# Kernel tuning notes

Measured on AMD Instinct MI355X. Metric: run time of the kernel, lower is better.

The kernel has to match this reference:

```python
import jax, jax.numpy as jnp
import numpy as np

N, D, K, MAX_ITER = 131072, 64, 512, 5


def setup_inputs() -> dict:
    key = jax.random.key(0)
    k1, k2, k3 = jax.random.split(key, 3)
    X = jax.random.normal(k1, (N, D), dtype=jnp.float32)
    centers = jax.random.normal(k2, (K, D), dtype=jnp.float32)
    repl_idx = jax.random.randint(k3, (MAX_ITER, K), 0, N, dtype=jnp.int32)
    return {"X": X, "centers": centers, "repl_idx": repl_idx}


def _assign(X, centers):
    # squared euclidean distance matrix [N, K]; argmin identical to cdist argmin
    x2 = jnp.sum(X * X, axis=1, keepdims=True)          # [N,1]
    c2 = jnp.sum(centers * centers, axis=1)             # [K]
    d2 = x2 + c2[None, :] - 2.0 * (X @ centers.T)       # [N,K]
    return jnp.argmin(d2, axis=1)


def reference(X, centers, repl_idx):
    n_clusters = centers.shape[0]
    assignments = None
    for i in range(MAX_ITER):
        assignments = _assign(X, centers)
        # scatter_mean: per-cluster sum / count (empty clusters -> 0, as torch_scatter)
        sums = jax.ops.segment_sum(X, assignments, num_segments=n_clusters)
        counts = jax.ops.segment_sum(jnp.ones((X.shape[0],), X.dtype), assignments,
                                     num_segments=n_clusters)
        new_centers = sums / jnp.maximum(counts, 1.0)[:, None]
        # re-initialize any exactly-zero entries from random data points
        new_centers_init = X[repl_idx[i]]                 # [K,D]
        new_centers = jnp.where(new_centers == 0, new_centers_init, new_centers)
        centers = new_centers
    return assignments, centers
```

## Files before the change

### kernel.cpp

```cpp
#include <hip/hip_runtime.h>

#define N_PTS 131072
#define KC    512
#define DIM   64
#define MAXIT 5
#define NCHUNK 64
#define CHUNK_PTS (N_PTS / NCHUNK)
#define FIXSCALE 1099511627776.0

typedef short v8s __attribute__((ext_vector_type(8)));
typedef float v4f __attribute__((ext_vector_type(4)));

__device__ __forceinline__ unsigned short bf16_rtne(float x) {
    unsigned int u = __float_as_uint(x);
    return (unsigned short)((u + 0x7FFFu + ((u >> 16) & 1u)) >> 16);
}
__device__ __forceinline__ float bf16_f32(unsigned short b) {
    return __uint_as_float(((unsigned int)b) << 16);
}
__device__ __forceinline__ void split3(float x, short& h, short& m, short& l) {
    unsigned short hb = bf16_rtne(x);
    float r1 = x - bf16_f32(hb);
    unsigned short mb = bf16_rtne(r1);
    float r2 = r1 - bf16_f32(mb);
    h = (short)hb; m = (short)mb; l = (short)bf16_rtne(r2);
}

__device__ __forceinline__ void gload_lds16(const unsigned short* g, void* lds) {
    __builtin_amdgcn_global_load_lds(
        (const __attribute__((address_space(1))) void*)g,
        (__attribute__((address_space(3))) void*)lds,
        16, 0, 0);
}

__global__ __launch_bounds__(256) void prep_kernel(
        const float* __restrict__ C, float* __restrict__ c2out,
        unsigned short* __restrict__ Ch, unsigned short* __restrict__ Cm,
        unsigned short* __restrict__ Cl) {
    int k = blockIdx.x * 256 + threadIdx.x;
    if (k < KC) {
        float sq[DIM];
        #pragma unroll
        for (int j = 0; j < DIM; ++j) {
            float c = C[k * DIM + j];
            sq[j] = c * c;
            short h, m, l;
            split3(c, h, m, l);
            Ch[k * DIM + j] = (unsigned short)h;
            Cm[k * DIM + j] = (unsigned short)m;
            Cl[k * DIM + j] = (unsigned short)l;
        }
        #pragma unroll
        for (int st = 1; st < DIM; st <<= 1)
            #pragma unroll
            for (int j = 0; j < DIM; j += 2 * st)
                sq[j] = sq[j] + sq[j + st];
        c2out[k] = sq[0];
    }
}

__global__ __launch_bounds__(256, 4) void assign_kernel(
        const float* __restrict__ X,
        const unsigned short* __restrict__ Ch,
        const unsigned short* __restrict__ Cm,
        const unsigned short* __restrict__ Cl,
        const float* __restrict__ c2v, float* __restrict__ out_f) {
    __shared__ __align__(16) short Bt[2 * 6 * 64 * 8];
    __shared__ float c2t[KC];
    __shared__ float x2p[4][2][16][8];
    __shared__ float x2f[4][2][16];

    const int t   = threadIdx.x;
    const int wv  = t >> 6;
    const int l   = t & 63;
    const int row = l & 15;
    const int q   = l >> 4;
    const int pbase = blockIdx.x * 128 + wv * 32;

    const unsigned short* const gsrc1 =
        ((wv < 2) ? Ch : Cm) + (size_t)(row * 64 + (wv & 1) * 32 + q * 8);
    const unsigned short* const gsrc2 =
        Cl + (size_t)(row * 64 + wv * 32 + q * 8);

    v8s* const BtV = (v8s*)Bt;
    v8s* const lds1 = BtV + wv * 64;
    v8s* const lds2 = BtV + 256 + wv * 64;

    gload_lds16(gsrc1, lds1);
    if (wv < 2) gload_lds16(gsrc2, lds2);

    for (int i = t; i < KC; i += 256) c2t[i] = c2v[i];

    v8s ah[2][2], am[2][2], al[2][2];
    #pragma unroll
    for (int T = 0; T < 2; ++T) {
        const float* xr = X + (size_t)(pbase + T * 16 + row) * DIM + q * 8;
        #pragma unroll
        for (int kc = 0; kc < 2; ++kc) {
            float4 v0 = *(const float4*)(xr + kc * 32);
            float4 v1 = *(const float4*)(xr + kc * 32 + 4);
            float e[8] = { v0.x, v0.y, v0.z, v0.w, v1.x, v1.y, v1.z, v1.w };
            v8s H, M, L;
            #pragma unroll
            for (int j = 0; j < 8; ++j) {
                short hh, mm, ll;
                split3(e[j], hh, mm, ll);
                H[j] = hh; M[j] = mm; L[j] = ll;
            }
            ah[T][kc] = H; am[T][kc] = M; al[T][kc] = L;
            float s0 = e[0]*e[0], s1 = e[1]*e[1], s2 = e[2]*e[2], s3 = e[3]*e[3];
            float s4 = e[4]*e[4], s5 = e[5]*e[5], s6 = e[6]*e[6], s7 = e[7]*e[7];
            x2p[wv][T][row][kc * 4 + q] =
                ((s0 + s1) + (s2 + s3)) + ((s4 + s5) + (s6 + s7));
        }
    }
    __syncthreads();
    if (t < 128) {
        int w2 = t >> 5, T2 = (t >> 4) & 1, pt = t & 15;
        const float* P = x2p[w2][T2][pt];
        x2f[w2][T2][pt] = ((P[0] + P[1]) + (P[2] + P[3]))
                        + ((P[4] + P[5]) + (P[6] + P[7]));
    }
    __syncthreads();
    float x2x[2][4];
    #pragma unroll
    for (int T = 0; T < 2; ++T)
        #pragma unroll
        for (int r = 0; r < 4; ++r)
            x2x[T][r] = x2f[wv][T][q * 4 + r];

    float bd[2][4];
    int   bk[2][4];
    #pragma unroll
    for (int T = 0; T < 2; ++T)
        #pragma unroll
        for (int r = 0; r < 4; ++r) { bd[T][r] = 3.4e38f; bk[T][r] = 0; }

    for (int ct = 0; ct < 32; ++ct) {
        const int cur = ct & 1;
        if (ct < 31) {
            const size_t goff = (size_t)(ct + 1) * 1024;
            gload_lds16(gsrc1 + goff, lds1 + (cur ^ 1) * 384);
            if (wv < 2) gload_lds16(gsrc2 + goff, lds2 + (cur ^ 1) * 384);
        }
        v8s* const rb = BtV + cur * 384;
        v8s bh0 = rb[0 * 64 + l];
        v8s bh1 = rb[1 * 64 + l];
        v8s bm0 = rb[2 * 64 + l];
        v8s bm1 = rb[3 * 64 + l];
        v8s bl0 = rb[4 * 64 + l];
        v8s bl1 = rb[5 * 64 + l];
        float c2k = c2t[ct * 16 + row];

        #pragma unroll
        for (int T = 0; T < 2; ++T) {
            v4f acc = {0.f, 0.f, 0.f, 0.f};
            acc = __builtin_amdgcn_mfma_f32_16x16x32_bf16(ah[T][0], bh0, acc, 0, 0, 0);
            acc = __builtin_amdgcn_mfma_f32_16x16x32_bf16(ah[T][1], bh1, acc, 0, 0, 0);
            acc = __builtin_amdgcn_mfma_f32_16x16x32_bf16(am[T][0], bh0, acc, 0, 0, 0);
            acc = __builtin_amdgcn_mfma_f32_16x16x32_bf16(am[T][1], bh1, acc, 0, 0, 0);
            acc = __builtin_amdgcn_mfma_f32_16x16x32_bf16(ah[T][0], bm0, acc, 0, 0, 0);
            acc = __builtin_amdgcn_mfma_f32_16x16x32_bf16(ah[T][1], bm1, acc, 0, 0, 0);
            acc = __builtin_amdgcn_mfma_f32_16x16x32_bf16(am[T][0], bm0, acc, 0, 0, 0);
            acc = __builtin_amdgcn_mfma_f32_16x16x32_bf16(am[T][1], bm1, acc, 0, 0, 0);
            acc = __builtin_amdgcn_mfma_f32_16x16x32_bf16(al[T][0], bh0, acc, 0, 0, 0);
            acc = __builtin_amdgcn_mfma_f32_16x16x32_bf16(al[T][1], bh1, acc, 0, 0, 0);
            acc = __builtin_amdgcn_mfma_f32_16x16x32_bf16(ah[T][0], bl0, acc, 0, 0, 0);
            acc = __builtin_amdgcn_mfma_f32_16x16x32_bf16(ah[T][1], bl1, acc, 0, 0, 0);
            #pragma unroll
            for (int r = 0; r < 4; ++r) {
                float tt = x2x[T][r] + c2k;
                float d2 = fmaf(-2.0f, acc[r], tt);
                if (d2 < bd[T][r]) { bd[T][r] = d2; bk[T][r] = ct * 16 + row; }
            }
        }
        if (ct < 31) __syncthreads();
    }

    #pragma unroll
    for (int T = 0; T < 2; ++T)
        #pragma unroll
        for (int r = 0; r < 4; ++r) {
            unsigned int b = __float_as_uint(bd[T][r]);
            b = (b & 0x80000000u) ? ~b : (b | 0x80000000u);
            unsigned long long key = ((unsigned long long)b << 32)
                                   | (unsigned int)bk[T][r];
            #pragma unroll
            for (int st = 1; st <= 8; st <<= 1) {
                unsigned long long o = __shfl_xor(key, st, 64);
                if (o < key) key = o;
            }
            if (row == 0) {
                int p = pbase + T * 16 + q * 4 + r;
                out_f[p] = (float)((int)(unsigned int)key);
            }
        }
}

__global__ __launch_bounds__(256) void accum_kernel(
        const float* __restrict__ X, const float* __restrict__ af,
        unsigned long long* __restrict__ qsums, int* __restrict__ counts) {
    __shared__ unsigned long long lsum[KC * 16];
    __shared__ int lcnt[KC];
    int slice = blockIdx.x & 3;
    int chunk = blockIdx.x >> 2;
    int p4 = threadIdx.x >> 2;
    int c4 = threadIdx.x & 3;

    for (int i = threadIdx.x; i < KC * 16; i += 256) lsum[i] = 0ull;
    for (int i = threadIdx.x; i < KC; i += 256) lcnt[i] = 0;
    __syncthreads();

    int base = chunk * CHUNK_PTS;
    #pragma unroll 2
    for (int it = 0; it < CHUNK_PTS / 64; ++it) {
        int n = base + it * 64 + p4;
        int a = (int)af[n];
        float4 xv = *(const float4*)(X + (size_t)n * DIM + slice * 16 + c4 * 4);
        long long q0 = (long long)llrint((double)xv.x * FIXSCALE);
        long long q1 = (long long)llrint((double)xv.y * FIXSCALE);
        long long q2 = (long long)llrint((double)xv.z * FIXSCALE);
        long long q3 = (long long)llrint((double)xv.w * FIXSCALE);
        atomicAdd(&lsum[a * 16 + c4 * 4 + 0], (unsigned long long)q0);
        atomicAdd(&lsum[a * 16 + c4 * 4 + 1], (unsigned long long)q1);
        atomicAdd(&lsum[a * 16 + c4 * 4 + 2], (unsigned long long)q2);
        atomicAdd(&lsum[a * 16 + c4 * 4 + 3], (unsigned long long)q3);
        if (slice == 0 && c4 == 0) atomicAdd(&lcnt[a], 1);
    }
    __syncthreads();

    for (int i = threadIdx.x; i < KC * 16; i += 256) {
        unsigned long long v = lsum[i];
        if (v != 0ull)
            atomicAdd(&qsums[(i >> 4) * DIM + slice * 16 + (i & 15)], v);
    }
    if (slice == 0)
        for (int i = threadIdx.x; i < KC; i += 256) {
            int v = lcnt[i];
            if (v != 0) atomicAdd(&counts[i], v);
        }
}

__global__ __launch_bounds__(256) void update_kernel(
        const unsigned long long* __restrict__ qsums,
        const int* __restrict__ counts,
        const int* __restrict__ repl, const float* __restrict__ X,
        float* __restrict__ outC, float* __restrict__ c2v,
        unsigned short* __restrict__ Ch, unsigned short* __restrict__ Cm,
        unsigned short* __restrict__ Cl) {
    int k = blockIdx.x * 4 + (threadIdx.x >> 6);
    int d = threadIdx.x & 63;

    long long qq = (long long)qsums[k * DIM + d];
    float s = (float)((double)qq * (1.0 / FIXSCALE));
    float cnt = (float)counts[k];
    float v = s / fmaxf(cnt, 1.0f);
    if (v == 0.0f) v = X[(size_t)repl[k] * DIM + d];
    outC[k * DIM + d] = v;

    short h, m, l;
    split3(v, h, m, l);
    Ch[k * DIM + d] = (unsigned short)h;
    Cm[k * DIM + d] = (unsigned short)m;
    Cl[k * DIM + d] = (unsigned short)l;

    float sq = v * v;
    #pragma unroll
    for (int st = 1; st < 64; st <<= 1)
        sq += __shfl_xor(sq, st, 64);
    if (d == 0) c2v[k] = sq;
}

extern "C" void kernel_launch(void* const* d_in, const int* in_sizes, int n_in,
                              void* d_out, int out_size, void* d_ws, size_t ws_size,
                              hipStream_t stream) {
    const float* X    = (const float*)d_in[0];
    const float* C0   = (const float*)d_in[1];
    const int*   repl = (const int*)d_in[2];
    float* out = (float*)d_out;

    char* ws = (char*)d_ws;
    unsigned short* Ch = (unsigned short*)(ws + 0);
    unsigned short* Cm = (unsigned short*)(ws + (64 << 10));
    unsigned short* Cl = (unsigned short*)(ws + (128 << 10));
    unsigned long long* qsums = (unsigned long long*)(ws + (192 << 10));
    int*   counts = (int*)  (ws + (448 << 10));
    float* c2v    = (float*)(ws + (450 << 10));

    prep_kernel<<<2, 256, 0, stream>>>(C0, c2v, Ch, Cm, Cl);

    for (int i = 0; i < MAXIT; ++i) {
        assign_kernel<<<N_PTS / 128, 256, 0, stream>>>(
            X, Ch, Cm, Cl, c2v, out);

        hipMemsetAsync(qsums, 0, KC * DIM * sizeof(unsigned long long)
                                 + KC * sizeof(int), stream);

        accum_kernel<<<NCHUNK * 4, 256, 0, stream>>>(X, out, qsums, counts);

        update_kernel<<<KC / 4, 256, 0, stream>>>(
            qsums, counts, repl + i * KC, X, out + N_PTS, c2v, Ch, Cm, Cl);
    }
}
```

Baseline: 473.6 us.

## Use single-wave blocks with 64 points each and drop per-tile barriers

The assign kernel now launches 64-thread single-wavefront blocks, each handling 64 points (4 row tiles) instead of 4 waves of 32 points. Each wave loads all six centroid split planes into its own double-buffered LDS and waits on vmcnt instead of a block-wide __syncthreads per centroid tile. Every staged centroid tile is reused across twice as many point rows, and intra-block barriers go away. In exchange each wave issues more global-to-LDS traffic per point, per-block LDS use stays the same with fewer waves sharing it, and register pressure rises with the larger accumulator and operand arrays.

```diff
diff --git a/kernel.cpp b/kernel.cpp
--- a/kernel.cpp
+++ b/kernel.cpp
@@ -26,11 +26,10 @@
     h = (short)hb; m = (short)mb; l = (short)bf16_rtne(r2);
 }
 
-__device__ __forceinline__ void gload_lds16(const unsigned short* g, void* lds) {
+__device__ __forceinline__ void gl16(const unsigned short* g, void* lds) {
     __builtin_amdgcn_global_load_lds(
         (const __attribute__((address_space(1))) void*)g,
-        (__attribute__((address_space(3))) void*)lds,
-        16, 0, 0);
+        (__attribute__((address_space(3))) void*)lds, 16, 0, 0);
 }
 
 __global__ __launch_bounds__(256) void prep_kernel(
@@ -59,7 +58,7 @@
     }
 }
 
-__global__ __launch_bounds__(256, 4) void assign_kernel(
+__global__ __launch_bounds__(64, 2) void assign_kernel(
         const float* __restrict__ X,
         const unsigned short* __restrict__ Ch,
         const unsigned short* __restrict__ Cm,
@@ -67,33 +66,34 @@
         const float* __restrict__ c2v, float* __restrict__ out_f) {
     __shared__ __align__(16) short Bt[2 * 6 * 64 * 8];
     __shared__ float c2t[KC];
-    __shared__ float x2p[4][2][16][8];
-    __shared__ float x2f[4][2][16];
-
-    const int t   = threadIdx.x;
-    const int wv  = t >> 6;
-    const int l   = t & 63;
+    __shared__ float x2p[4][16][8];
+    __shared__ float x2f[4][16];
+
+    const int l   = threadIdx.x;
     const int row = l & 15;
     const int q   = l >> 4;
-    const int pbase = blockIdx.x * 128 + wv * 32;
-
-    const unsigned short* const gsrc1 =
-        ((wv < 2) ? Ch : Cm) + (size_t)(row * 64 + (wv & 1) * 32 + q * 8);
-    const unsigned short* const gsrc2 =
-        Cl + (size_t)(row * 64 + wv * 32 + q * 8);
+    const int pbase = blockIdx.x * 64;
+
+    const size_t boff = (size_t)(row * 64 + q * 8);
+    const unsigned short* ph  = Ch + boff;
+    const unsigned short* pm  = Cm + boff;
+    const unsigned short* plo = Cl + boff;
 
     v8s* const BtV = (v8s*)Bt;
-    v8s* const lds1 = BtV + wv * 64;
-    v8s* const lds2 = BtV + 256 + wv * 64;
-
-    gload_lds16(gsrc1, lds1);
-    if (wv < 2) gload_lds16(gsrc2, lds2);
-
-    for (int i = t; i < KC; i += 256) c2t[i] = c2v[i];
-
-    v8s ah[2][2], am[2][2], al[2][2];
-    #pragma unroll
-    for (int T = 0; T < 2; ++T) {
+
+    gl16(ph,       BtV + 0);
+    gl16(ph  + 32, BtV + 64);
+    gl16(pm,       BtV + 128);
+    gl16(pm  + 32, BtV + 192);
+    gl16(plo,      BtV + 256);
+    gl16(plo + 32, BtV + 320);
+    ph += 1024; pm += 1024; plo += 1024;
+
+    for (int i = l; i < KC; i += 64) c2t[i] = c2v[i];
+
+    v8s ah[4][2], am[4][2], al[4][2];
+    #pragma unroll
+    for (int T = 0; T < 4; ++T) {
         const float* xr = X + (size_t)(pbase + T * 16 + row) * DIM + q * 8;
         #pragma unroll
         for (int kc = 0; kc < 2; ++kc) {
@@ -110,40 +110,47 @@
             ah[T][kc] = H; am[T][kc] = M; al[T][kc] = L;
             float s0 = e[0]*e[0], s1 = e[1]*e[1], s2 = e[2]*e[2], s3 = e[3]*e[3];
             float s4 = e[4]*e[4], s5 = e[5]*e[5], s6 = e[6]*e[6], s7 = e[7]*e[7];
-            x2p[wv][T][row][kc * 4 + q] =
+            x2p[T][row][kc * 4 + q] =
                 ((s0 + s1) + (s2 + s3)) + ((s4 + s5) + (s6 + s7));
         }
     }
     __syncthreads();
-    if (t < 128) {
-        int w2 = t >> 5, T2 = (t >> 4) & 1, pt = t & 15;
-        const float* P = x2p[w2][T2][pt];
-        x2f[w2][T2][pt] = ((P[0] + P[1]) + (P[2] + P[3]))
-                        + ((P[4] + P[5]) + (P[6] + P[7]));
+    {
+        int T2 = l >> 4, pt = l & 15;
+        const float* P = x2p[T2][pt];
+        x2f[T2][pt] = ((P[0] + P[1]) + (P[2] + P[3]))
+                    + ((P[4] + P[5]) + (P[6] + P[7]));
     }
     __syncthreads();
-    float x2x[2][4];
-    #pragma unroll
-    for (int T = 0; T < 2; ++T)
+    float x2x[4][4];
+    #pragma unroll
+    for (int T = 0; T < 4; ++T)
         #pragma unroll
         for (int r = 0; r < 4; ++r)
-            x2x[T][r] = x2f[wv][T][q * 4 + r];
-
-    float bd[2][4];
-    int   bk[2][4];
-    #pragma unroll
-    for (int T = 0; T < 2; ++T)
+            x2x[T][r] = x2f[T][q * 4 + r];
+
+    float bd[4][4];
+    int   bk[4][4];
+    #pragma unroll
+    for (int T = 0; T < 4; ++T)
         #pragma unroll
         for (int r = 0; r < 4; ++r) { bd[T][r] = 3.4e38f; bk[T][r] = 0; }
 
     for (int ct = 0; ct < 32; ++ct) {
-        const int cur = ct & 1;
+        asm volatile("s_waitcnt vmcnt(0)" ::: "memory");
+        __builtin_amdgcn_sched_barrier(0);
         if (ct < 31) {
-            const size_t goff = (size_t)(ct + 1) * 1024;
-            gload_lds16(gsrc1 + goff, lds1 + (cur ^ 1) * 384);
-            if (wv < 2) gload_lds16(gsrc2 + goff, lds2 + (cur ^ 1) * 384);
-        }
-        v8s* const rb = BtV + cur * 384;
+            v8s* dst = BtV + ((ct + 1) & 1) * 384;
+            gl16(ph,       dst + 0);
+            gl16(ph  + 32, dst + 64);
+            gl16(pm,       dst + 128);
+            gl16(pm  + 32, dst + 192);
+            gl16(plo,      dst + 256);
+            gl16(plo + 32, dst + 320);
+            ph += 1024; pm += 1024; plo += 1024;
+        }
+        __builtin_amdgcn_sched_barrier(0);
+        const v8s* rb = BtV + (ct & 1) * 384;
         v8s bh0 = rb[0 * 64 + l];
         v8s bh1 = rb[1 * 64 + l];
         v8s bm0 = rb[2 * 64 + l];
@@ -153,7 +160,7 @@
         float c2k = c2t[ct * 16 + row];
 
         #pragma unroll
-        for (int T = 0; T < 2; ++T) {
+        for (int T = 0; T < 4; ++T) {
             v4f acc = {0.f, 0.f, 0.f, 0.f};
             acc = __builtin_amdgcn_mfma_f32_16x16x32_bf16(ah[T][0], bh0, acc, 0, 0, 0);
             acc = __builtin_amdgcn_mfma_f32_16x16x32_bf16(ah[T][1], bh1, acc, 0, 0, 0);
@@ -174,11 +181,10 @@
                 if (d2 < bd[T][r]) { bd[T][r] = d2; bk[T][r] = ct * 16 + row; }
             }
         }
-        if (ct < 31) __syncthreads();
-    }
-
-    #pragma unroll
-    for (int T = 0; T < 2; ++T)
+    }
+
+    #pragma unroll
+    for (int T = 0; T < 4; ++T)
         #pragma unroll
         for (int r = 0; r < 4; ++r) {
             unsigned int b = __float_as_uint(bd[T][r]);
@@ -290,7 +296,7 @@
     prep_kernel<<<2, 256, 0, stream>>>(C0, c2v, Ch, Cm, Cl);
 
     for (int i = 0; i < MAXIT; ++i) {
-        assign_kernel<<<N_PTS / 128, 256, 0, stream>>>(
+        assign_kernel<<<N_PTS / 64, 64, 0, stream>>>(
             X, Ch, Cm, Cl, c2v, out);
 
         hipMemsetAsync(qsums, 0, KC * DIM * sizeof(unsigned long long)
```

New measurement: 516.3 us. 9.0% more time.
